# Optimization experiments

Hardware: AMD Instinct MI355X
Metric: run time of the kernel (lower is better)

Reference implementation:

```python
import jax, jax.numpy as jnp
import numpy as np

EPS = 1e-7  # keras.backend.epsilon()
NUM_ROUTING = 3


def squash(v, axis=-1):
    s2 = jnp.sum(jnp.square(v), axis=axis, keepdims=True)
    scale = s2 / (1.0 + s2) / jnp.sqrt(s2 + EPS)
    return scale * v


def setup_inputs() -> dict:
    key = jax.random.key(0)
    k1, k2 = jax.random.split(key)
    B, N_in, C, d_in, d_out = 64, 4096, 10, 8, 16
    x = jax.random.normal(k1, (B, N_in, d_in), dtype=jnp.float32)
    # glorot-ish scale for transformation weights [N_in, C, d_in, d_out]
    W = jax.random.normal(k2, (N_in, C, d_in, d_out), dtype=jnp.float32) * (1.0 / np.sqrt(d_in + d_out))
    return {"x": x, "W": W}


def reference(x, W):
    # u_hat[b,n,c,e] = sum_d x[b,n,d] * W[n,c,d,e]  -- the tile+multiply+reduce in the original
    u_hat = jnp.einsum('bnd,ncde->bnce', x, W)  # [B, N_in, C, d_out]
    B, N_in, C, _ = u_hat.shape
    b = jnp.zeros((B, N_in, C), dtype=u_hat.dtype)
    v = None
    for i in range(NUM_ROUTING):
        c = jax.nn.softmax(b, axis=2)                    # [B, N_in, C]
        s = jnp.einsum('bnc,bnce->bce', c, u_hat)        # [B, C, d_out]
        v = squash(s)                                    # [B, C, d_out]
        if i < NUM_ROUTING - 1:
            agreement = jnp.einsum('bnce,bce->bnc', u_hat, v)
            b = b + agreement
    return v
```

## Files before the change

### kernel.cpp

```cpp
#include <hip/hip_runtime.h>
#include <hip/hip_fp16.h>

#define B_ 64
#define N_ 4096
#define C_ 10
#define D_ 8
#define E_ 16
#define EPS_ 1e-7f
#define NT_ 8
#define NBLK_ (N_ / NT_)
#define NSLOT_ NBLK_
#define PROW_ 80
#define WBROW_ 82
#define NSG_ 8

typedef _Float16 h2_t __attribute__((ext_vector_type(2)));
typedef __fp16   p2_t __attribute__((ext_vector_type(2)));

__device__ inline unsigned pkh(float a, float b) {
    p2_t t = __builtin_amdgcn_cvt_pkrtz(a, b);
    return *(unsigned*)&t;
}
#if __has_builtin(__builtin_amdgcn_fdot2)
__device__ inline float fd2(unsigned a, unsigned b, float c) {
    h2_t av = *(h2_t*)&a, bv = *(h2_t*)&b;
    return __builtin_amdgcn_fdot2(av, bv, c, false);
}
#else
__device__ inline float fd2(unsigned a, unsigned b, float c) {
    h2_t av = *(h2_t*)&a, bv = *(h2_t*)&b;
    return fmaf((float)av.x, (float)bv.x, fmaf((float)av.y, (float)bv.y, c));
}
#endif
__device__ inline float hlo(unsigned u) { h2_t t = *(h2_t*)&u; return (float)t.x; }
__device__ inline float hhi(unsigned u) { h2_t t = *(h2_t*)&u; return (float)t.y; }
__device__ inline unsigned hpack(float a, float b) {
    __half2 t = __floats2half2_rn(a, b);
    return *(unsigned*)&t;
}
__device__ inline float2 hunpack(unsigned u) {
    return __half22float2(*(const __half2*)&u);
}

template <bool UNIFORM>
__global__ __launch_bounds__(512, 4) void caps_pass(
    const float* __restrict__ x, const float* __restrict__ W,
    const unsigned* __restrict__ vpk, unsigned* __restrict__ partial)
{
    __shared__ __align__(16) char smem[30720];
    uint4*    wlds = (uint4*)smem;
    unsigned* xlds = (unsigned*)(smem + 20480);
    float*    xch  = (float*)(smem + 28672);
    unsigned* wb   = (unsigned*)smem;

    const int tid = (int)threadIdx.x;
    const int blk = (int)blockIdx.x;
    const int n0  = blk * NT_;

    {
        const float4* wg = (const float4*)W + (size_t)blk * (NT_ * 320);
#pragma unroll
        for (int k = 0; k < 3; ++k) {
            const int g = k * 512 + tid;
            if (g < NT_ * C_ * 16) {
                const int n   = g / 160;
                const int rem = g - n * 160;
                const int c   = rem >> 4;
                const int r2  = rem & 15;
                const int d2  = r2 >> 2;
                const int eqs = r2 & 3;
                const float4 g0 = wg[n * 320 + c * 32 + (2 * d2) * 4 + eqs];
                const float4 g1 = wg[n * 320 + c * 32 + (2 * d2 + 1) * 4 + eqs];
                wlds[((n * C_ + c) * 4 + d2) * 4 + eqs] =
                    make_uint4(pkh(g0.x, g1.x), pkh(g0.y, g1.y),
                               pkh(g0.z, g1.z), pkh(g0.w, g1.w));
            }
        }
    }
    {
        const float4* xg = (const float4*)x;
#pragma unroll
        for (int k = 0; k < 2; ++k) {
            const int g = k * 512 + tid;
            const int b = g >> 4;
            const int r = g & 15;
            const int n = r >> 1;
            const int dq = r & 1;
            const float4 v = xg[((size_t)b * N_ + n0 + n) * 2 + dq];
            *(uint2*)&xlds[(n * B_ + b) * 4 + dq * 2] =
                make_uint2(pkh(v.x, v.y), pkh(v.z, v.w));
        }
    }
    __syncthreads();

    const int wv   = tid >> 6;
    const int lane = tid & 63;
    const int eq   = lane & 3;
    const int bl   = lane >> 2;
    const int h    = wv & 1;
    const int cg   = (wv >> 1) & 1;
    const int np   = wv >> 2;
    const int b0   = h * 32 + bl;
    const int b1   = b0 + 16;
    const int cbase = cg * 5;
    float* xme = xch + (((cg) * 4 + np * 2 + h) * 16 + bl) * 2;
    float* xot = xch + (((cg ^ 1) * 4 + np * 2 + h) * 16 + bl) * 2;

    unsigned vcp0[5][2], vcp1[5][2];
    if (!UNIFORM) {
#pragma unroll
        for (int cc = 0; cc < 5; ++cc) {
            const int c = cbase + cc;
            const uint2 a = *(const uint2*)(vpk + (b0 * C_ + c) * 8 + eq * 2);
            vcp0[cc][0] = a.x; vcp0[cc][1] = a.y;
            const uint2 d = *(const uint2*)(vpk + (b1 * C_ + c) * 8 + eq * 2);
            vcp1[cc][0] = d.x; vcp1[cc][1] = d.y;
        }
    }

    float4 acc0[5], acc1[5];
#pragma unroll
    for (int cc = 0; cc < 5; ++cc) {
        acc0[cc] = make_float4(0.f, 0.f, 0.f, 0.f);
        acc1[cc] = make_float4(0.f, 0.f, 0.f, 0.f);
    }

#pragma unroll 1
    for (int j = 0; j < 4; ++j) {
        const int nl = np * 4 + j;
        const uint4 xq0 = *(const uint4*)&xlds[(nl * B_ + b0) * 4];
        const uint4 xq1 = *(const uint4*)&xlds[(nl * B_ + b1) * 4];
        const unsigned xa[4] = {xq0.x, xq0.y, xq0.z, xq0.w};
        const unsigned xb[4] = {xq1.x, xq1.y, xq1.z, xq1.w};

        if (UNIFORM) {
#pragma unroll
            for (int cc = 0; cc < 5; ++cc) {
                const uint4* wq = &wlds[(nl * C_ + cbase + cc) * 16];
#pragma unroll
                for (int d2 = 0; d2 < 4; ++d2) {
                    const uint4 q = wq[d2 * 4 + eq];
                    acc0[cc].x = fd2(xa[d2], q.x, acc0[cc].x);
                    acc0[cc].y = fd2(xa[d2], q.y, acc0[cc].y);
                    acc0[cc].z = fd2(xa[d2], q.z, acc0[cc].z);
                    acc0[cc].w = fd2(xa[d2], q.w, acc0[cc].w);
                    acc1[cc].x = fd2(xb[d2], q.x, acc1[cc].x);
                    acc1[cc].y = fd2(xb[d2], q.y, acc1[cc].y);
                    acc1[cc].z = fd2(xb[d2], q.z, acc1[cc].z);
                    acc1[cc].w = fd2(xb[d2], q.w, acc1[cc].w);
                }
            }
        } else {
            unsigned uhp0[5][2], uhp1[5][2];
            float wgt0[5], wgt1[5];
            float s0 = 0.f, s1 = 0.f;
#pragma unroll
            for (int cc = 0; cc < 5; ++cc) {
                const uint4* wq = &wlds[(nl * C_ + cbase + cc) * 16];
                float4 u0 = make_float4(0.f, 0.f, 0.f, 0.f);
                float4 u1 = make_float4(0.f, 0.f, 0.f, 0.f);
#pragma unroll
                for (int d2 = 0; d2 < 4; ++d2) {
                    const uint4 q = wq[d2 * 4 + eq];
                    u0.x = fd2(xa[d2], q.x, u0.x);
                    u0.y = fd2(xa[d2], q.y, u0.y);
                    u0.z = fd2(xa[d2], q.z, u0.z);
                    u0.w = fd2(xa[d2], q.w, u0.w);
                    u1.x = fd2(xb[d2], q.x, u1.x);
                    u1.y = fd2(xb[d2], q.y, u1.y);
                    u1.z = fd2(xb[d2], q.z, u1.z);
                    u1.w = fd2(xb[d2], q.w, u1.w);
                }
                const unsigned up00 = pkh(u0.x, u0.y), up01 = pkh(u0.z, u0.w);
                const unsigned up10 = pkh(u1.x, u1.y), up11 = pkh(u1.z, u1.w);
                float t0 = fd2(up00, vcp0[cc][0], fd2(up01, vcp0[cc][1], 0.f));
                t0 += __shfl_xor(t0, 1); t0 += __shfl_xor(t0, 2);
                float t1 = fd2(up10, vcp1[cc][0], fd2(up11, vcp1[cc][1], 0.f));
                t1 += __shfl_xor(t1, 1); t1 += __shfl_xor(t1, 2);
                wgt0[cc] = __expf(t0); s0 += wgt0[cc];
                wgt1[cc] = __expf(t1); s1 += wgt1[cc];
                uhp0[cc][0] = up00; uhp0[cc][1] = up01;
                uhp1[cc][0] = up10; uhp1[cc][1] = up11;
            }
            if (eq == 0) { xme[0] = s0; xme[1] = s1; }
            __syncthreads();
            const float i0 = 1.f / (s0 + xot[0]);
            const float i1 = 1.f / (s1 + xot[1]);
#pragma unroll
            for (int cc = 0; cc < 5; ++cc) {
                const float g0 = wgt0[cc] * i0, g1 = wgt1[cc] * i1;
                acc0[cc].x = fmaf(g0, hlo(uhp0[cc][0]), acc0[cc].x);
                acc0[cc].y = fmaf(g0, hhi(uhp0[cc][0]), acc0[cc].y);
                acc0[cc].z = fmaf(g0, hlo(uhp0[cc][1]), acc0[cc].z);
                acc0[cc].w = fmaf(g0, hhi(uhp0[cc][1]), acc0[cc].w);
                acc1[cc].x = fmaf(g1, hlo(uhp1[cc][0]), acc1[cc].x);
                acc1[cc].y = fmaf(g1, hhi(uhp1[cc][0]), acc1[cc].y);
                acc1[cc].z = fmaf(g1, hlo(uhp1[cc][1]), acc1[cc].z);
                acc1[cc].w = fmaf(g1, hhi(uhp1[cc][1]), acc1[cc].w);
            }
        }
    }

    const float fold = UNIFORM ? 0.1f : 1.f;
    __syncthreads();
    if (np == 1) {
#pragma unroll
        for (int cc = 0; cc < 5; ++cc) {
            const int c = cbase + cc;
            *(uint2*)&wb[b0 * WBROW_ + c * 8 + eq * 2] =
                make_uint2(hpack(acc0[cc].x * fold, acc0[cc].y * fold),
                           hpack(acc0[cc].z * fold, acc0[cc].w * fold));
            *(uint2*)&wb[b1 * WBROW_ + c * 8 + eq * 2] =
                make_uint2(hpack(acc1[cc].x * fold, acc1[cc].y * fold),
                           hpack(acc1[cc].z * fold, acc1[cc].w * fold));
        }
    }
    __syncthreads();
    if (np == 0) {
#pragma unroll
        for (int cc = 0; cc < 5; ++cc) {
            const int c = cbase + cc;
            const uint2 p0 = *(const uint2*)&wb[b0 * WBROW_ + c * 8 + eq * 2];
            const float2 a0 = hunpack(p0.x), a1 = hunpack(p0.y);
            *(uint2*)(partial + ((size_t)b0 * NSLOT_ + blk) * PROW_ + c * 8 + eq * 2) =
                make_uint2(hpack(a0.x + acc0[cc].x * fold, a0.y + acc0[cc].y * fold),
                           hpack(a1.x + acc0[cc].z * fold, a1.y + acc0[cc].w * fold));
            const uint2 p1 = *(const uint2*)&wb[b1 * WBROW_ + c * 8 + eq * 2];
            const float2 d0 = hunpack(p1.x), d1 = hunpack(p1.y);
            *(uint2*)(partial + ((size_t)b1 * NSLOT_ + blk) * PROW_ + c * 8 + eq * 2) =
                make_uint2(hpack(d0.x + acc1[cc].x * fold, d0.y + acc1[cc].y * fold),
                           hpack(d1.x + acc1[cc].z * fold, d1.y + acc1[cc].w * fold));
        }
    }
}

__global__ __launch_bounds__(256) void caps_redA(
    const unsigned* __restrict__ partial, float* __restrict__ sub)
{
    const int b  = (int)blockIdx.x >> 3;
    const int sg = (int)blockIdx.x & 7;
    const int tid = (int)threadIdx.x;
    const int sc   = tid >> 5;
    const int col4 = tid & 31;
    __shared__ float red[8][20][8];
    if (col4 < 20) {
        float s[8];
#pragma unroll
        for (int p = 0; p < 8; ++p) s[p] = 0.f;
        const int slot0 = sg * (NSLOT_ / NSG_) + sc * 8;
        const uint4* base = (const uint4*)(partial +
            ((size_t)b * NSLOT_ + slot0) * PROW_) + col4;
#pragma unroll 4
        for (int k = 0; k < 8; ++k) {
            const uint4 q = base[k * (PROW_ / 4)];
            const float2 f0 = hunpack(q.x), f1 = hunpack(q.y);
            const float2 f2 = hunpack(q.z), f3 = hunpack(q.w);
            s[0] += f0.x; s[1] += f0.y; s[2] += f1.x; s[3] += f1.y;
            s[4] += f2.x; s[5] += f2.y; s[6] += f3.x; s[7] += f3.y;
        }
#pragma unroll
        for (int p = 0; p < 8; ++p) red[sc][col4][p] = s[p];
    }
    __syncthreads();
    if (tid < 160) {
        const int c4 = tid >> 3, p = tid & 7;
        float s = 0.f;
#pragma unroll
        for (int ch = 0; ch < 8; ++ch) s += red[ch][c4][p];
        sub[((size_t)b * NSG_ + sg) * (C_ * E_) + c4 * 8 + p] = s;
    }
}

__global__ __launch_bounds__(128) void caps_redB(
    const float* __restrict__ sub, float* __restrict__ v_cum,
    unsigned* __restrict__ vpk, float* __restrict__ out, int mode)
{
    const int b = (int)blockIdx.x;
    const int tid = (int)threadIdx.x;
    if (tid >= PROW_) return;
    float slo = 0.f, shi = 0.f;
#pragma unroll
    for (int sg = 0; sg < NSG_; ++sg) {
        const float* p = sub + ((size_t)b * NSG_ + sg) * (C_ * E_) + tid * 2;
        slo += p[0]; shi += p[1];
    }
    float p = slo * slo + shi * shi;
    p += __shfl_xor(p, 1); p += __shfl_xor(p, 2); p += __shfl_xor(p, 4);
    const float sc = (p / (1.f + p)) * rsqrtf(p + EPS_);
    float v0 = sc * slo, v1 = sc * shi;
    const int o = b * (C_ * E_) + tid * 2;
    if (mode == 2) {
        out[o] = v0; out[o + 1] = v1;
    } else {
        if (mode == 0) {
            v_cum[o] = v0; v_cum[o + 1] = v1;
        } else {
            v0 += v_cum[o]; v1 += v_cum[o + 1];
            v_cum[o] = v0; v_cum[o + 1] = v1;
        }
        vpk[b * PROW_ + tid] = hpack(v0, v1);
    }
}

extern "C" void kernel_launch(void* const* d_in, const int* in_sizes, int n_in,
                              void* d_out, int out_size, void* d_ws, size_t ws_size,
                              hipStream_t stream) {
    const float* x = (const float*)d_in[0];
    const float* W = (const float*)d_in[1];
    float* out = (float*)d_out;

    char* p = (char*)d_ws;
    unsigned* partial = (unsigned*)p;
    p += (size_t)B_ * NSLOT_ * PROW_ * sizeof(unsigned);
    float* sub = (float*)p;
    p += (size_t)B_ * NSG_ * C_ * E_ * sizeof(float);
    float* v_cum = (float*)p;
    p += (size_t)B_ * C_ * E_ * sizeof(float);
    unsigned* vpk = (unsigned*)p;

    for (int t = 0; t < 3; ++t) {
        if (t == 0)
            caps_pass<true ><<<dim3(NBLK_), 512, 0, stream>>>(x, W, vpk, partial);
        else
            caps_pass<false><<<dim3(NBLK_), 512, 0, stream>>>(x, W, vpk, partial);
        caps_redA<<<dim3(B_ * NSG_), 256, 0, stream>>>(partial, sub);
        caps_redB<<<dim3(B_), 128, 0, stream>>>(sub, v_cum, vpk, out, t);
    }
}
```

Measured before the change: 78.12 us.

## Halve block size and give each thread four batch rows for more W reuse

Each caps_pass block now runs 256 threads instead of 512, and every thread computes four batch rows instead of two. Each W value read from LDS is reused across more FMAs, which cuts LDS traffic per flop. The softmax-denominator exchange buffer is now double-buffered by j parity, which suits the single barrier per iteration. The cost is more registers per thread (acc[4][5] float4, plus uhp and wgt arrays), which could lower occupancy or cause spills under launch_bounds(256,2).

```diff
diff --git a/kernel.cpp b/kernel.cpp
--- a/kernel.cpp
+++ b/kernel.cpp
@@ -43,7 +43,7 @@
 }
 
 template <bool UNIFORM>
-__global__ __launch_bounds__(512, 4) void caps_pass(
+__global__ __launch_bounds__(256, 2) void caps_pass(
     const float* __restrict__ x, const float* __restrict__ W,
     const unsigned* __restrict__ vpk, unsigned* __restrict__ partial)
 {
@@ -60,28 +60,26 @@
     {
         const float4* wg = (const float4*)W + (size_t)blk * (NT_ * 320);
 #pragma unroll
-        for (int k = 0; k < 3; ++k) {
-            const int g = k * 512 + tid;
-            if (g < NT_ * C_ * 16) {
-                const int n   = g / 160;
-                const int rem = g - n * 160;
-                const int c   = rem >> 4;
-                const int r2  = rem & 15;
-                const int d2  = r2 >> 2;
-                const int eqs = r2 & 3;
-                const float4 g0 = wg[n * 320 + c * 32 + (2 * d2) * 4 + eqs];
-                const float4 g1 = wg[n * 320 + c * 32 + (2 * d2 + 1) * 4 + eqs];
-                wlds[((n * C_ + c) * 4 + d2) * 4 + eqs] =
-                    make_uint4(pkh(g0.x, g1.x), pkh(g0.y, g1.y),
-                               pkh(g0.z, g1.z), pkh(g0.w, g1.w));
-            }
+        for (int k = 0; k < 5; ++k) {
+            const int g = k * 256 + tid;
+            const int n   = g / 160;
+            const int rem = g - n * 160;
+            const int c   = rem >> 4;
+            const int r2  = rem & 15;
+            const int d2  = r2 >> 2;
+            const int eqs = r2 & 3;
+            const float4 g0 = wg[n * 320 + c * 32 + (2 * d2) * 4 + eqs];
+            const float4 g1 = wg[n * 320 + c * 32 + (2 * d2 + 1) * 4 + eqs];
+            wlds[((n * C_ + c) * 4 + d2) * 4 + eqs] =
+                make_uint4(pkh(g0.x, g1.x), pkh(g0.y, g1.y),
+                           pkh(g0.z, g1.z), pkh(g0.w, g1.w));
         }
     }
     {
         const float4* xg = (const float4*)x;
 #pragma unroll
-        for (int k = 0; k < 2; ++k) {
-            const int g = k * 512 + tid;
+        for (int k = 0; k < 4; ++k) {
+            const int g = k * 256 + tid;
             const int b = g >> 4;
             const int r = g & 15;
             const int n = r >> 1;
@@ -97,41 +95,39 @@
     const int lane = tid & 63;
     const int eq   = lane & 3;
     const int bl   = lane >> 2;
-    const int h    = wv & 1;
-    const int cg   = (wv >> 1) & 1;
-    const int np   = wv >> 2;
-    const int b0   = h * 32 + bl;
-    const int b1   = b0 + 16;
+    const int cg   = wv & 1;
+    const int np   = wv >> 1;
     const int cbase = cg * 5;
-    float* xme = xch + (((cg) * 4 + np * 2 + h) * 16 + bl) * 2;
-    float* xot = xch + (((cg ^ 1) * 4 + np * 2 + h) * 16 + bl) * 2;
-
-    unsigned vcp0[5][2], vcp1[5][2];
+
+    unsigned vcp[4][5][2];
     if (!UNIFORM) {
 #pragma unroll
-        for (int cc = 0; cc < 5; ++cc) {
-            const int c = cbase + cc;
-            const uint2 a = *(const uint2*)(vpk + (b0 * C_ + c) * 8 + eq * 2);
-            vcp0[cc][0] = a.x; vcp0[cc][1] = a.y;
-            const uint2 d = *(const uint2*)(vpk + (b1 * C_ + c) * 8 + eq * 2);
-            vcp1[cc][0] = d.x; vcp1[cc][1] = d.y;
-        }
-    }
-
-    float4 acc0[5], acc1[5];
-#pragma unroll
-    for (int cc = 0; cc < 5; ++cc) {
-        acc0[cc] = make_float4(0.f, 0.f, 0.f, 0.f);
-        acc1[cc] = make_float4(0.f, 0.f, 0.f, 0.f);
-    }
+        for (int i = 0; i < 4; ++i) {
+            const int b = bl + i * 16;
+#pragma unroll
+            for (int cc = 0; cc < 5; ++cc) {
+                const uint2 a = *(const uint2*)(vpk + (b * C_ + cbase + cc) * 8 + eq * 2);
+                vcp[i][cc][0] = a.x; vcp[i][cc][1] = a.y;
+            }
+        }
+    }
+
+    float4 acc[4][5];
+#pragma unroll
+    for (int i = 0; i < 4; ++i)
+#pragma unroll
+        for (int cc = 0; cc < 5; ++cc)
+            acc[i][cc] = make_float4(0.f, 0.f, 0.f, 0.f);
 
 #pragma unroll 1
     for (int j = 0; j < 4; ++j) {
         const int nl = np * 4 + j;
-        const uint4 xq0 = *(const uint4*)&xlds[(nl * B_ + b0) * 4];
-        const uint4 xq1 = *(const uint4*)&xlds[(nl * B_ + b1) * 4];
-        const unsigned xa[4] = {xq0.x, xq0.y, xq0.z, xq0.w};
-        const unsigned xb[4] = {xq1.x, xq1.y, xq1.z, xq1.w};
+        unsigned xa[4][4];
+#pragma unroll
+        for (int i = 0; i < 4; ++i) {
+            const uint4 xq = *(const uint4*)&xlds[(nl * B_ + bl + i * 16) * 4];
+            xa[i][0] = xq.x; xa[i][1] = xq.y; xa[i][2] = xq.z; xa[i][3] = xq.w;
+        }
 
         if (UNIFORM) {
 #pragma unroll
@@ -140,63 +136,62 @@
 #pragma unroll
                 for (int d2 = 0; d2 < 4; ++d2) {
                     const uint4 q = wq[d2 * 4 + eq];
-                    acc0[cc].x = fd2(xa[d2], q.x, acc0[cc].x);
-                    acc0[cc].y = fd2(xa[d2], q.y, acc0[cc].y);
-                    acc0[cc].z = fd2(xa[d2], q.z, acc0[cc].z);
-                    acc0[cc].w = fd2(xa[d2], q.w, acc0[cc].w);
-                    acc1[cc].x = fd2(xb[d2], q.x, acc1[cc].x);
-                    acc1[cc].y = fd2(xb[d2], q.y, acc1[cc].y);
-                    acc1[cc].z = fd2(xb[d2], q.z, acc1[cc].z);
-                    acc1[cc].w = fd2(xb[d2], q.w, acc1[cc].w);
+#pragma unroll
+                    for (int i = 0; i < 4; ++i) {
+                        acc[i][cc].x = fd2(xa[i][d2], q.x, acc[i][cc].x);
+                        acc[i][cc].y = fd2(xa[i][d2], q.y, acc[i][cc].y);
+                        acc[i][cc].z = fd2(xa[i][d2], q.z, acc[i][cc].z);
+                        acc[i][cc].w = fd2(xa[i][d2], q.w, acc[i][cc].w);
+                    }
                 }
             }
         } else {
-            unsigned uhp0[5][2], uhp1[5][2];
-            float wgt0[5], wgt1[5];
-            float s0 = 0.f, s1 = 0.f;
+            unsigned uhp[4][5][2];
+            float wgt[4][5];
+            float s[4] = {0.f, 0.f, 0.f, 0.f};
 #pragma unroll
             for (int cc = 0; cc < 5; ++cc) {
                 const uint4* wq = &wlds[(nl * C_ + cbase + cc) * 16];
-                float4 u0 = make_float4(0.f, 0.f, 0.f, 0.f);
-                float4 u1 = make_float4(0.f, 0.f, 0.f, 0.f);
+                float4 u[4];
+#pragma unroll
+                for (int i = 0; i < 4; ++i) u[i] = make_float4(0.f, 0.f, 0.f, 0.f);
 #pragma unroll
                 for (int d2 = 0; d2 < 4; ++d2) {
                     const uint4 q = wq[d2 * 4 + eq];
-                    u0.x = fd2(xa[d2], q.x, u0.x);
-                    u0.y = fd2(xa[d2], q.y, u0.y);
-                    u0.z = fd2(xa[d2], q.z, u0.z);
-                    u0.w = fd2(xa[d2], q.w, u0.w);
-                    u1.x = fd2(xb[d2], q.x, u1.x);
-                    u1.y = fd2(xb[d2], q.y, u1.y);
-                    u1.z = fd2(xb[d2], q.z, u1.z);
-                    u1.w = fd2(xb[d2], q.w, u1.w);
+#pragma unroll
+                    for (int i = 0; i < 4; ++i) {
+                        u[i].x = fd2(xa[i][d2], q.x, u[i].x);
+                        u[i].y = fd2(xa[i][d2], q.y, u[i].y);
+                        u[i].z = fd2(xa[i][d2], q.z, u[i].z);
+                        u[i].w = fd2(xa[i][d2], q.w, u[i].w);
+                    }
                 }
-                const unsigned up00 = pkh(u0.x, u0.y), up01 = pkh(u0.z, u0.w);
-                const unsigned up10 = pkh(u1.x, u1.y), up11 = pkh(u1.z, u1.w);
-                float t0 = fd2(up00, vcp0[cc][0], fd2(up01, vcp0[cc][1], 0.f));
-                t0 += __shfl_xor(t0, 1); t0 += __shfl_xor(t0, 2);
-                float t1 = fd2(up10, vcp1[cc][0], fd2(up11, vcp1[cc][1], 0.f));
-                t1 += __shfl_xor(t1, 1); t1 += __shfl_xor(t1, 2);
-                wgt0[cc] = __expf(t0); s0 += wgt0[cc];
-                wgt1[cc] = __expf(t1); s1 += wgt1[cc];
-                uhp0[cc][0] = up00; uhp0[cc][1] = up01;
-                uhp1[cc][0] = up10; uhp1[cc][1] = up11;
-            }
-            if (eq == 0) { xme[0] = s0; xme[1] = s1; }
+#pragma unroll
+                for (int i = 0; i < 4; ++i) {
+                    const unsigned up0 = pkh(u[i].x, u[i].y);
+                    const unsigned up1 = pkh(u[i].z, u[i].w);
+                    float t = fd2(up0, vcp[i][cc][0], fd2(up1, vcp[i][cc][1], 0.f));
+                    t += __shfl_xor(t, 1); t += __shfl_xor(t, 2);
+                    const float e = __expf(t);
+                    wgt[i][cc] = e; s[i] += e;
+                    uhp[i][cc][0] = up0; uhp[i][cc][1] = up1;
+                }
+            }
+            float* xme = xch + ((((j & 1) * 2 + cg) * 2 + np) * 16 + bl) * 4;
+            const float* xot = xch + ((((j & 1) * 2 + (cg ^ 1)) * 2 + np) * 16 + bl) * 4;
+            if (eq == 0) *(float4*)xme = make_float4(s[0], s[1], s[2], s[3]);
             __syncthreads();
-            const float i0 = 1.f / (s0 + xot[0]);
-            const float i1 = 1.f / (s1 + xot[1]);
-#pragma unroll
-            for (int cc = 0; cc < 5; ++cc) {
-                const float g0 = wgt0[cc] * i0, g1 = wgt1[cc] * i1;
-                acc0[cc].x = fmaf(g0, hlo(uhp0[cc][0]), acc0[cc].x);
-                acc0[cc].y = fmaf(g0, hhi(uhp0[cc][0]), acc0[cc].y);
-                acc0[cc].z = fmaf(g0, hlo(uhp0[cc][1]), acc0[cc].z);
-                acc0[cc].w = fmaf(g0, hhi(uhp0[cc][1]), acc0[cc].w);
-                acc1[cc].x = fmaf(g1, hlo(uhp1[cc][0]), acc1[cc].x);
-                acc1[cc].y = fmaf(g1, hhi(uhp1[cc][0]), acc1[cc].y);
-                acc1[cc].z = fmaf(g1, hlo(uhp1[cc][1]), acc1[cc].z);
-                acc1[cc].w = fmaf(g1, hhi(uhp1[cc][1]), acc1[cc].w);
+#pragma unroll
+            for (int i = 0; i < 4; ++i) {
+                const float inv = 1.f / (s[i] + xot[i]);
+#pragma unroll
+                for (int cc = 0; cc < 5; ++cc) {
+                    const float g = wgt[i][cc] * inv;
+                    acc[i][cc].x = fmaf(g, hlo(uhp[i][cc][0]), acc[i][cc].x);
+                    acc[i][cc].y = fmaf(g, hhi(uhp[i][cc][0]), acc[i][cc].y);
+                    acc[i][cc].z = fmaf(g, hlo(uhp[i][cc][1]), acc[i][cc].z);
+                    acc[i][cc].w = fmaf(g, hhi(uhp[i][cc][1]), acc[i][cc].w);
+                }
             }
         }
     }
@@ -205,31 +200,31 @@
     __syncthreads();
     if (np == 1) {
 #pragma unroll
-        for (int cc = 0; cc < 5; ++cc) {
-            const int c = cbase + cc;
-            *(uint2*)&wb[b0 * WBROW_ + c * 8 + eq * 2] =
-                make_uint2(hpack(acc0[cc].x * fold, acc0[cc].y * fold),
-                           hpack(acc0[cc].z * fold, acc0[cc].w * fold));
-            *(uint2*)&wb[b1 * WBROW_ + c * 8 + eq * 2] =
-                make_uint2(hpack(acc1[cc].x * fold, acc1[cc].y * fold),
-                           hpack(acc1[cc].z * fold, acc1[cc].w * fold));
+        for (int i = 0; i < 4; ++i) {
+            const int b = bl + i * 16;
+#pragma unroll
+            for (int cc = 0; cc < 5; ++cc) {
+                const int c = cbase + cc;
+                *(uint2*)&wb[b * WBROW_ + c * 8 + eq * 2] =
+                    make_uint2(hpack(acc[i][cc].x * fold, acc[i][cc].y * fold),
+                               hpack(acc[i][cc].z * fold, acc[i][cc].w * fold));
+            }
         }
     }
     __syncthreads();
     if (np == 0) {
 #pragma unroll
-        for (int cc = 0; cc < 5; ++cc) {
-            const int c = cbase + cc;
-            const uint2 p0 = *(const uint2*)&wb[b0 * WBROW_ + c * 8 + eq * 2];
-            const float2 a0 = hunpack(p0.x), a1 = hunpack(p0.y);
-            *(uint2*)(partial + ((size_t)b0 * NSLOT_ + blk) * PROW_ + c * 8 + eq * 2) =
-                make_uint2(hpack(a0.x + acc0[cc].x * fold, a0.y + acc0[cc].y * fold),
-                           hpack(a1.x + acc0[cc].z * fold, a1.y + acc0[cc].w * fold));
-            const uint2 p1 = *(const uint2*)&wb[b1 * WBROW_ + c * 8 + eq * 2];
-            const float2 d0 = hunpack(p1.x), d1 = hunpack(p1.y);
-            *(uint2*)(partial + ((size_t)b1 * NSLOT_ + blk) * PROW_ + c * 8 + eq * 2) =
-                make_uint2(hpack(d0.x + acc1[cc].x * fold, d0.y + acc1[cc].y * fold),
-                           hpack(d1.x + acc1[cc].z * fold, d1.y + acc1[cc].w * fold));
+        for (int i = 0; i < 4; ++i) {
+            const int b = bl + i * 16;
+#pragma unroll
+            for (int cc = 0; cc < 5; ++cc) {
+                const int c = cbase + cc;
+                const uint2 p0 = *(const uint2*)&wb[b * WBROW_ + c * 8 + eq * 2];
+                const float2 a0 = hunpack(p0.x), a1 = hunpack(p0.y);
+                *(uint2*)(partial + ((size_t)b * NSLOT_ + blk) * PROW_ + c * 8 + eq * 2) =
+                    make_uint2(hpack(a0.x + acc[i][cc].x * fold, a0.y + acc[i][cc].y * fold),
+                               hpack(a1.x + acc[i][cc].z * fold, a1.y + acc[i][cc].w * fold));
+            }
         }
     }
 }
@@ -320,9 +315,9 @@
 
     for (int t = 0; t < 3; ++t) {
         if (t == 0)
-            caps_pass<true ><<<dim3(NBLK_), 512, 0, stream>>>(x, W, vpk, partial);
+            caps_pass<true ><<<dim3(NBLK_), 256, 0, stream>>>(x, W, vpk, partial);
         else
-            caps_pass<false><<<dim3(NBLK_), 512, 0, stream>>>(x, W, vpk, partial);
+            caps_pass<false><<<dim3(NBLK_), 256, 0, stream>>>(x, W, vpk, partial);
         caps_redA<<<dim3(B_ * NSG_), 256, 0, stream>>>(partial, sub);
         caps_redB<<<dim3(B_), 128, 0, stream>>>(sub, v_cum, vpk, out, t);
     }
```

After: 79.42 us. Within noise of the previous version (+1.7%).
